# Optimization experiments

Hardware: AMD Instinct MI355X
Metric: run time of the kernel (lower is better)

The kernel has to match this reference:

```python
import jax, jax.numpy as jnp
import numpy as np

B, S, DIM = 1, 2048, 2048
H = 16
Q_LORA, KV_LORA = 1536, 512
D_NOPE, D_ROPE, D_V = 128, 64, 128
D_QK = D_NOPE + D_ROPE  # 192
EPS = 1e-6


def rms_norm(x, w, eps=EPS):
    var = jnp.mean(jnp.square(x), axis=-1, keepdims=True)
    return x * jax.lax.rsqrt(var + eps) * w


def apply_rope(x, cos, sin):
    # x: [B,S,H,D] with interleaved complex pairs; cos/sin: [S,D//2]
    x1, x2 = x[..., 0::2], x[..., 1::2]
    c = cos[None, :, None, :]
    s = sin[None, :, None, :]
    o1 = x1 * c - x2 * s
    o2 = x1 * s + x2 * c
    return jnp.stack([o1, o2], axis=-1).reshape(x.shape)


def setup_inputs() -> dict:
    key = jax.random.key(0)
    ks = jax.random.split(key, 8)
    x = jax.random.normal(ks[0], (B, S, DIM), dtype=jnp.float32)
    # rotary tables (standard complex exponentials)
    inv_freq = 1.0 / (10000.0 ** (np.arange(0, D_ROPE, 2, dtype=np.float32) / D_ROPE))
    t = np.arange(S, dtype=np.float32)
    freqs = np.outer(t, inv_freq)  # [S, D_ROPE//2]
    freqs_cos = jnp.asarray(np.cos(freqs))
    freqs_sin = jnp.asarray(np.sin(freqs))
    sd = lambda fan_in: 1.0 / np.sqrt(fan_in)
    wq_a = jax.random.normal(ks[1], (Q_LORA, DIM), dtype=jnp.float32) * sd(DIM)
    q_a_ln_w = jnp.ones((Q_LORA,), dtype=jnp.float32)
    wq_b = jax.random.normal(ks[2], (H * D_QK, Q_LORA), dtype=jnp.float32) * sd(Q_LORA)
    wkv_a = jax.random.normal(ks[3], (KV_LORA + D_ROPE, DIM), dtype=jnp.float32) * sd(DIM)
    kv_a_ln_w = jnp.ones((KV_LORA,), dtype=jnp.float32)
    wkv_b = jax.random.normal(ks[4], (H * (D_NOPE + D_V), KV_LORA), dtype=jnp.float32) * sd(KV_LORA)
    wo = jax.random.normal(ks[5], (DIM, H * D_V), dtype=jnp.float32) * sd(H * D_V)
    return {"x": x, "freqs_cos": freqs_cos, "freqs_sin": freqs_sin,
            "wq_a": wq_a, "q_a_ln_w": q_a_ln_w, "wq_b": wq_b,
            "wkv_a": wkv_a, "kv_a_ln_w": kv_a_ln_w, "wkv_b": wkv_b, "wo": wo}


def reference(x, freqs_cos, freqs_sin, wq_a, q_a_ln_w, wq_b, wkv_a, kv_a_ln_w, wkv_b, wo):
    softmax_scale = D_QK ** -0.5
    # Query: low-rank down-proj -> RMSNorm -> up-proj
    q = rms_norm(x @ wq_a.T, q_a_ln_w) @ wq_b.T            # [B,S,H*D_QK]
    q = q.reshape(B, S, H, D_QK)
    q_nope, q_pe = q[..., :D_NOPE], q[..., D_NOPE:]
    q_pe = apply_rope(q_pe, freqs_cos, freqs_sin)
    # KV: shared low-rank latent + decoupled rope key (MQA-style, 1 head)
    kv = x @ wkv_a.T                                        # [B,S,KV_LORA+D_ROPE]
    kv_c = rms_norm(kv[..., :KV_LORA], kv_a_ln_w)           # [B,S,KV_LORA]
    k_pe = apply_rope(kv[..., None, KV_LORA:], freqs_cos, freqs_sin)  # [B,S,1,D_ROPE]
    kvb = (kv_c @ wkv_b.T).reshape(B, S, H, D_NOPE + D_V)
    k_nope, v = kvb[..., :D_NOPE], kvb[..., D_NOPE:]
    # Attention scores: nope part + shared rope part
    scores = (jnp.einsum('bqhd,bkhd->bhqk', q_nope, k_nope)
              + jnp.einsum('bqhd,bkd->bhqk', q_pe, k_pe[:, :, 0, :])) * softmax_scale
    causal = jnp.tril(jnp.ones((S, S), dtype=bool))
    scores = jnp.where(causal[None, None], scores, -jnp.inf)
    p = jax.nn.softmax(scores, axis=-1)
    out = jnp.einsum('bhqk,bkhd->bqhd', p, v).reshape(B, S, H * D_V)
    return out @ wo.T
```

## Files before the change

kernel.cpp:

```cpp
#include <hip/hip_runtime.h>
#include <cstdint>
#include <cstddef>

typedef __bf16 bf16;
typedef bf16 bf16x8 __attribute__((ext_vector_type(8)));
typedef bf16 bf16x4 __attribute__((ext_vector_type(4)));
typedef float f32x4 __attribute__((ext_vector_type(4)));

typedef __attribute__((address_space(1))) void as1_void;
typedef __attribute__((address_space(3))) void as3_void;

#define INF __builtin_inff()

__global__ __launch_bounds__(256) void z100_cast_all(
    const float* __restrict__ x, const float* __restrict__ wq_a,
    const float* __restrict__ wkv_a, const float* __restrict__ wq_b,
    const float* __restrict__ wkv_b, const float* __restrict__ wo,
    bf16* __restrict__ x_bf, bf16* __restrict__ wab_bf,
    bf16* __restrict__ wqb_bf, bf16* __restrict__ wkvb_bf,
    bf16* __restrict__ wo_bf) {
    int i = blockIdx.x * 256 + threadIdx.x;
    const float* s;
    bf16* d;
    if (i < 1048576)      { s = x + (size_t)i * 4;                     d = x_bf + (size_t)i * 4; }
    else if (i < 1835008) { int o = i - 1048576; s = wq_a  + (size_t)o * 4; d = wab_bf + (size_t)o * 4; }
    else if (i < 2129920) { int o = i - 1835008; s = wkv_a + (size_t)o * 4; d = wab_bf + 1536ull * 2048 + (size_t)o * 4; }
    else if (i < 3309568) { int o = i - 2129920; s = wq_b  + (size_t)o * 4; d = wqb_bf + (size_t)o * 4; }
    else if (i < 3833856) { int o = i - 3309568; s = wkv_b + (size_t)o * 4; d = wkvb_bf + (size_t)o * 4; }
    else if (i < 4882432) { int o = i - 3833856; s = wo    + (size_t)o * 4; d = wo_bf + (size_t)o * 4; }
    else {                  int o = i - 4882432; bf16x4 z = {};
                            *(bf16x4*)(wab_bf + 2112ull * 2048 + (size_t)o * 4) = z; return; }
    float4 v = *(const float4*)s;
    bf16x4 ovec = { (bf16)v.x, (bf16)v.y, (bf16)v.z, (bf16)v.w };
    *(bf16x4*)d = ovec;
}

__global__ __launch_bounds__(256) void z100_rmsnorm(
    const float* __restrict__ x, int ldx, const float* __restrict__ w,
    bf16* __restrict__ y, int N, float invN) {
    const int row = blockIdx.x;
    const float* xr = x + (size_t)row * ldx;
    float ss = 0.f;
    for (int i = threadIdx.x * 4; i < N; i += 1024) {
        float4 v = *(const float4*)(xr + i);
        ss += v.x * v.x + v.y * v.y + v.z * v.z + v.w * v.w;
    }
    #pragma unroll
    for (int d = 1; d < 64; d <<= 1) ss += __shfl_xor(ss, d);
    __shared__ float red[4];
    if ((threadIdx.x & 63) == 0) red[threadIdx.x >> 6] = ss;
    __syncthreads();
    float tot = red[0] + red[1] + red[2] + red[3];
    float rs = rsqrtf(tot * invN + 1e-6f);
    bf16* yr = y + (size_t)row * N;
    for (int i = threadIdx.x * 4; i < N; i += 1024) {
        float4 v = *(const float4*)(xr + i);
        float4 wv = *(const float4*)(w + i);
        bf16x4 o = { (bf16)(v.x * rs * wv.x), (bf16)(v.y * rs * wv.y),
                     (bf16)(v.z * rs * wv.z), (bf16)(v.w * rs * wv.w) };
        *(bf16x4*)(yr + i) = o;
    }
}

template <typename OutT>
__device__ __forceinline__ void gemm8_body(
    const bf16* __restrict__ A, const bf16* __restrict__ B,
    OutT* __restrict__ C, int N, int K, int ldc, int mblk, int nblk,
    bf16* AsB, bf16* BsB) {
    const int tid = threadIdx.x;
    const int lane = tid & 63, wave = tid >> 6;
    const int l15 = lane & 15, l4 = lane >> 4;
    const int m0 = mblk * 128, n0 = nblk * 128;
    const int wr = (wave >> 1) * 32, wc = (wave & 1) * 64;

    f32x4 acc[2][4] = {};

    const int srow = lane >> 2;
    const int scol = (lane & 3) * 8;
    const size_t a_base = (size_t)(m0 + wave * 16 + srow) * K + scol;
    const size_t b_base = (size_t)(n0 + wave * 16 + srow) * K + scol;

    auto stg = [&](int buf, int k0) {
        __builtin_amdgcn_global_load_lds((as1_void*)(void*)(A + a_base + k0),
                                         (as3_void*)(AsB + buf * 4096 + wave * 512), 16, 0, 0);
        __builtin_amdgcn_global_load_lds((as1_void*)(void*)(B + b_base + k0),
                                         (as3_void*)(BsB + buf * 4096 + wave * 512), 16, 0, 0);
    };

    const int nt = K >> 5;
    stg(0, 0);
    stg(1, 32);
    asm volatile("s_waitcnt vmcnt(2)" ::: "memory");
    __builtin_amdgcn_s_barrier();

    int cb = 0, sb = 2;
    for (int t = 0; t < nt; ++t) {
        if (t + 2 < nt) stg(sb, (t + 2) * 32);
        const bf16* Ab = AsB + cb * 4096;
        const bf16* Bb = BsB + cb * 4096;
        bf16x8 fa[2], fb[4];
        #pragma unroll
        for (int i = 0; i < 2; ++i)
            fa[i] = *(const bf16x8*)(Ab + (wr + 16 * i + l15) * 32 + 8 * l4);
        #pragma unroll
        for (int j = 0; j < 4; ++j)
            fb[j] = *(const bf16x8*)(Bb + (wc + 16 * j + l15) * 32 + 8 * l4);
        #pragma unroll
        for (int i = 0; i < 2; ++i)
            #pragma unroll
            for (int j = 0; j < 4; ++j)
                acc[i][j] = __builtin_amdgcn_mfma_f32_16x16x32_bf16(fa[i], fb[j], acc[i][j], 0, 0, 0);
        if (t + 2 < nt) { asm volatile("s_waitcnt vmcnt(2)" ::: "memory"); }
        else            { asm volatile("s_waitcnt vmcnt(0)" ::: "memory"); }
        __builtin_amdgcn_s_barrier();
        cb = (cb == 2) ? 0 : cb + 1;
        sb = (sb == 2) ? 0 : sb + 1;
    }

    #pragma unroll
    for (int i = 0; i < 2; ++i) {
        int row0 = m0 + wr + 16 * i + 4 * l4;
        #pragma unroll
        for (int j = 0; j < 4; ++j) {
            int col = n0 + wc + 16 * j + l15;
            if (col < N) {
                #pragma unroll
                for (int jj = 0; jj < 4; ++jj)
                    C[(size_t)(row0 + jj) * ldc + col] = (OutT)acc[i][j][jj];
            }
        }
    }
}

__global__ __launch_bounds__(512) void z100_gemm8(
    const bf16* __restrict__ A, const bf16* __restrict__ B,
    float* __restrict__ C, int N, int K, int ldc) {
    __shared__ alignas(16) bf16 As[3 * 128 * 32];
    __shared__ alignas(16) bf16 Bs[3 * 128 * 32];
    gemm8_body<float>(A, B, C, N, K, ldc, blockIdx.y, blockIdx.x, As, Bs);
}

__global__ __launch_bounds__(512) void z100_gemm_qkv(
    const bf16* __restrict__ qan, const bf16* __restrict__ wqb, bf16* __restrict__ qf,
    const bf16* __restrict__ kvc, const bf16* __restrict__ wkvb, bf16* __restrict__ kvbf) {
    __shared__ alignas(16) bf16 As[3 * 128 * 32];
    __shared__ alignas(16) bf16 Bs[3 * 128 * 32];
    const int bid = blockIdx.x;
    if (bid < 384) gemm8_body<bf16>(qan, wqb, qf, 3072, 1536, 3072, bid / 24, bid % 24, As, Bs);
    else { int b = bid - 384; gemm8_body<bf16>(kvc, wkvb, kvbf, 4096, 512, 4096, b / 32, b % 32, As, Bs); }
}

__global__ void z100_qk_prep(const bf16* __restrict__ q,
                             const bf16* __restrict__ kvb, const float* __restrict__ kpe,
                             int kpe_ld,
                             const float* __restrict__ fc, const float* __restrict__ fs,
                             bf16* __restrict__ q_attn, bf16* __restrict__ k_attn) {
    const int TOT = 2048 * 16 * 96;
    int u = blockIdx.x * 256 + threadIdx.x;
    if (u < TOT) {
        int e = u % 96;
        int sh = u / 96;
        int h = sh % 16, s = sh / 16;
        const float scale = 0.072168783649f;
        const bf16* qp = q + (size_t)s * 3072 + h * 192;
        bf16* o = q_attn + ((size_t)h * 2048 + s) * 192;
        if (e < 64) {
            o[2 * e]     = (bf16)((float)qp[2 * e] * scale);
            o[2 * e + 1] = (bf16)((float)qp[2 * e + 1] * scale);
        } else {
            int i = e - 64;
            float c = fc[s * 32 + i], sn = fs[s * 32 + i];
            float x1 = (float)qp[128 + 2 * i], x2 = (float)qp[128 + 2 * i + 1];
            o[128 + 2 * i]     = (bf16)((x1 * c - x2 * sn) * scale);
            o[128 + 2 * i + 1] = (bf16)((x1 * sn + x2 * c) * scale);
        }
    } else {
        u -= TOT;
        int e = u % 96;
        int sh = u / 96;
        int h = sh % 16, s = sh / 16;
        bf16* o = k_attn + ((size_t)h * 2048 + s) * 192;
        if (e < 64) {
            const bf16* kp = kvb + (size_t)s * 4096 + h * 256;
            o[2 * e]     = kp[2 * e];
            o[2 * e + 1] = kp[2 * e + 1];
        } else {
            int i = e - 64;
            float c = fc[s * 32 + i], sn = fs[s * 32 + i];
            float x1 = kpe[(size_t)s * kpe_ld + 2 * i];
            float x2 = kpe[(size_t)s * kpe_ld + 2 * i + 1];
            o[128 + 2 * i]     = (bf16)(x1 * c - x2 * sn);
            o[128 + 2 * i + 1] = (bf16)(x1 * sn + x2 * c);
        }
    }
}

__global__ __launch_bounds__(256) void z100_v_trans(const bf16* __restrict__ kvb,
                                                    bf16* __restrict__ vt) {
    const int st = blockIdx.x, h = blockIdx.y;
    const int s0 = st * 64;
    __shared__ alignas(16) bf16 tile[64 * 132];
    const int tid = threadIdx.x;
    #pragma unroll
    for (int i = 0; i < 4; ++i) {
        int slot = i * 256 + tid;
        int r = slot >> 4, c8 = slot & 15;
        bf16x8 v = *(const bf16x8*)(kvb + (size_t)(s0 + r) * 4096 + h * 256 + 128 + c8 * 8);
        *(bf16x8*)(tile + r * 132 + c8 * 8) = v;
    }
    __syncthreads();
    #pragma unroll
    for (int i = 0; i < 4; ++i) {
        int slot = i * 256 + tid;
        int d = slot >> 3, ch = slot & 7;
        bf16x8 o;
        #pragma unroll
        for (int j = 0; j < 8; ++j) o[j] = tile[(ch * 8 + j) * 132 + d];
        *(bf16x8*)(vt + ((size_t)h * 128 + d) * 2048 + s0 + ch * 8) = o;
    }
}

__global__ __launch_bounds__(512) void z100_attn(
    const bf16* __restrict__ q_attn, const bf16* __restrict__ k_attn,
    const bf16* __restrict__ v_t, bf16* __restrict__ opart, float* __restrict__ ml) {
    const int bid = blockIdx.x;
    const int wk = (bid & 7) * 80 + (bid >> 3);
    const int h = wk / 40;
    const int s0w = wk - h * 40;
    int qt = 0, rem = s0w;
    while (rem >= (qt >> 2) + 1) { rem -= (qt >> 2) + 1; ++qt; }
    const int chk = rem;
    const int q0 = qt * 128;
    const int kstart = chk * 512;
    const int kend = min(q0 + 128, kstart + 512);
    const int slot = h * 40 + s0w;

    const int tid = threadIdx.x;
    const int lane = tid & 63, wave = tid >> 6;
    const int l15 = lane & 15, l4 = lane >> 4;

    __shared__ alignas(16) bf16 Ks[2][64 * 192];
    __shared__ alignas(16) bf16 Vs[2][128 * 64];

    const bf16* Qh = q_attn + (size_t)h * 2048 * 192;
    const bf16* Kh = k_attn + (size_t)h * 2048 * 192;
    const bf16* Vh = v_t + (size_t)h * 128 * 2048;

    const int wrow_max = q0 + wave * 16 + 15;
    const int diag_k0 = q0 + (wave >> 2) * 64;

    bf16x8 qf[6];
    {
        const bf16* qr = Qh + (size_t)(q0 + wave * 16 + l15) * 192 + 8 * l4;
        #pragma unroll
        for (int c = 0; c < 6; ++c) qf[c] = *(const bf16x8*)(qr + 32 * c);
    }

    int koff[3], voff[2];
    #pragma unroll
    for (int i = 0; i < 3; ++i) {
        int off = (wave * 3 + i) * 1024 + lane * 16;
        int r = off / 384;
        int ch = (off % 384) >> 4;
        int ksrc = (r & 0x23) | ((r & 0x0C) << 1) | ((r & 0x10) >> 2);
        koff[i] = ksrc * 192 + (ch ^ (r & 7)) * 8;
    }
    #pragma unroll
    for (int i = 0; i < 2; ++i) {
        int off = (wave * 2 + i) * 1024 + lane * 16;
        int d = off >> 7;
        int ch = (off >> 4) & 7;
        voff[i] = d * 2048 + (ch ^ (d & 7)) * 8;
    }

    auto stage = [&](int buf, int k0) {
        #pragma unroll
        for (int i = 0; i < 3; ++i)
            __builtin_amdgcn_global_load_lds(
                (as1_void*)(void*)(Kh + (size_t)k0 * 192 + koff[i]),
                (as3_void*)((char*)&Ks[buf][0] + (wave * 3 + i) * 1024), 16, 0, 0);
        #pragma unroll
        for (int i = 0; i < 2; ++i)
            __builtin_amdgcn_global_load_lds(
                (as1_void*)(void*)(Vh + k0 + voff[i]),
                (as3_void*)((char*)&Vs[buf][0] + (wave * 2 + i) * 1024), 16, 0, 0);
    };

    f32x4 oacc[8] = {};
    float m_r = -INF, l_r = 0.f;
    const int nt = (kend - kstart) >> 6;

    stage(0, kstart);
    __syncthreads();
    int cur = 0;
    for (int t = 0; t < nt; ++t) {
        const int k0 = kstart + t * 64;
        if (t + 1 < nt) stage(cur ^ 1, k0 + 64);

        if (k0 <= wrow_max) {
            const char* KsC = (const char*)&Ks[cur][0];
            const char* VsC = (const char*)&Vs[cur][0];

            f32x4 sc[4];
            __builtin_amdgcn_s_setprio(1);
            #pragma unroll
            for (int kt = 0; kt < 4; ++kt) {
                f32x4 a = { 0.f, 0.f, 0.f, 0.f };
                int r = 16 * kt + l15;
                #pragma unroll
                for (int c = 0; c < 6; ++c) {
                    int byteo = (r * 384 + c * 64 + l4 * 16) ^ ((r & 7) << 4);
                    bf16x8 kf = *(const bf16x8*)(KsC + byteo);
                    a = __builtin_amdgcn_mfma_f32_16x16x32_bf16(kf, qf[c], a, 0, 0, 0);
                }
                sc[kt] = a;
            }
            __builtin_amdgcn_s_setprio(0);

            if (k0 == diag_k0) {
                int qrow = (wave & 3) * 16 + l15;
                #pragma unroll
                for (int kt = 0; kt < 4; ++kt)
                    #pragma unroll
                    for (int r = 0; r < 4; ++r) {
                        int kl = ((kt >> 1) << 5) | (l4 << 3) | ((kt & 1) << 2) | r;
                        if (kl > qrow) sc[kt][r] = -INF;
                    }
            }

            float mx = -INF;
            #pragma unroll
            for (int kt = 0; kt < 4; ++kt)
                #pragma unroll
                for (int r = 0; r < 4; ++r) mx = fmaxf(mx, sc[kt][r]);
            mx = fmaxf(mx, __shfl_xor(mx, 16));
            mx = fmaxf(mx, __shfl_xor(mx, 32));
            float mnew = fmaxf(m_r, mx);
            float corr = __expf(m_r - mnew);
            float rs = 0.f;
            #pragma unroll
            for (int kt = 0; kt < 4; ++kt)
                #pragma unroll
                for (int r = 0; r < 4; ++r) {
                    float pv = __expf(sc[kt][r] - mnew);
                    sc[kt][r] = pv;
                    rs += pv;
                }
            rs += __shfl_xor(rs, 16);
            rs += __shfl_xor(rs, 32);
            l_r = l_r * corr + rs;
            m_r = mnew;

            float c_r[4];
            #pragma unroll
            for (int r = 0; r < 4; ++r) c_r[r] = __shfl(corr, 20 * l4 + r);
            #pragma unroll
            for (int dt = 0; dt < 8; ++dt)
                #pragma unroll
                for (int r = 0; r < 4; ++r) oacc[dt][r] *= c_r[r];

            bf16x8 pf[2];
            #pragma unroll
            for (int c2 = 0; c2 < 2; ++c2)
                #pragma unroll
                for (int i = 0; i < 8; ++i)
                    pf[c2][i] = (bf16)sc[2 * c2 + (i >> 2)][i & 3];

            __builtin_amdgcn_s_setprio(1);
            #pragma unroll
            for (int dt = 0; dt < 8; ++dt) {
                #pragma unroll
                for (int c2 = 0; c2 < 2; ++c2) {
                    int d = 16 * dt + l15;
                    int byteo = (d * 128 + c2 * 64 + l4 * 16) ^ ((d & 7) << 4);
                    bf16x8 vf = *(const bf16x8*)(VsC + byteo);
                    oacc[dt] = __builtin_amdgcn_mfma_f32_16x16x32_bf16(pf[c2], vf, oacc[dt], 0, 0, 0);
                }
            }
            __builtin_amdgcn_s_setprio(0);
        }

        __syncthreads();
        cur ^= 1;
    }

    const int qr_base = wave * 16;
    if (lane < 16) {
        ml[(size_t)slot * 256 + qr_base + lane] = m_r;
        ml[(size_t)slot * 256 + 128 + qr_base + lane] = l_r;
    }
    bf16* ob = opart + (size_t)slot * 16384;
    #pragma unroll
    for (int dt = 0; dt < 8; ++dt) {
        int d = 16 * dt + l15;
        #pragma unroll
        for (int r = 0; r < 4; ++r) {
            int qr = qr_base + 4 * l4 + r;
            ob[qr * 128 + d] = (bf16)oacc[dt][r];
        }
    }
}

__global__ __launch_bounds__(512) void z100_attn_combine(
    const bf16* __restrict__ opart, const float* __restrict__ ml, bf16* __restrict__ ao) {
    const int qt = blockIdx.x, h = blockIdx.y;
    const int t = threadIdx.x;
    const int np = (qt >> 2) + 1;
    int base = 0;
    for (int j = 0; j < qt; ++j) base += (j >> 2) + 1;
    const int slot0 = h * 40 + base;
    #pragma unroll 1
    for (int it = 0; it < 4; ++it) {
        const int c = it * 512 + t;
        const int qr = c >> 4;
        const int dc = (c & 15) * 8;
        float m[4], l[4], w[4];
        float M = -INF;
        #pragma unroll
        for (int i = 0; i < 4; ++i)
            if (i < np) {
                m[i] = ml[(size_t)(slot0 + i) * 256 + qr];
                l[i] = ml[(size_t)(slot0 + i) * 256 + 128 + qr];
                M = fmaxf(M, m[i]);
            }
        float L = 0.f;
        #pragma unroll
        for (int i = 0; i < 4; ++i)
            if (i < np) {
                w[i] = __expf(m[i] - M);
                L += w[i] * l[i];
            }
        float invL = 1.f / L;
        float acc[8] = {};
        #pragma unroll
        for (int i = 0; i < 4; ++i)
            if (i < np) {
                bf16x8 a = *(const bf16x8*)(opart + (size_t)(slot0 + i) * 16384 + (size_t)c * 8);
                #pragma unroll
                for (int j = 0; j < 8; ++j) acc[j] += w[i] * (float)a[j];
            }
        bf16x8 o;
        #pragma unroll
        for (int j = 0; j < 8; ++j) o[j] = (bf16)(acc[j] * invL);
        *(bf16x8*)(ao + (size_t)(qt * 128 + qr) * 2048 + h * 128 + dc) = o;
    }
}

extern "C" void kernel_launch(void* const* d_in, const int* in_sizes, int n_in,
                              void* d_out, int out_size, void* d_ws, size_t ws_size,
                              hipStream_t stream) {
    (void)in_sizes; (void)n_in; (void)out_size; (void)ws_size;
    const float* x     = (const float*)d_in[0];
    const float* fc    = (const float*)d_in[1];
    const float* fs    = (const float*)d_in[2];
    const float* wq_a  = (const float*)d_in[3];
    const float* q_ln  = (const float*)d_in[4];
    const float* wq_b  = (const float*)d_in[5];
    const float* wkv_a = (const float*)d_in[6];
    const float* kv_ln = (const float*)d_in[7];
    const float* wkv_b = (const float*)d_in[8];
    const float* wo    = (const float*)d_in[9];
    float* out = (float*)d_out;

    char* p = (char*)d_ws;
    auto alloc = [&](size_t bytes) {
        char* r = p;
        p += (bytes + 255) & ~(size_t)255;
        return r;
    };
    char* phase1  = p;
    bf16* x_bf    = (bf16*)alloc(2048ull * 2048 * 2);
    bf16* wab_bf  = (bf16*)alloc(2176ull * 2048 * 2);
    float* qa_f   = (float*)alloc(2048ull * 2112 * 4);
    bf16* qan_bf  = (bf16*)alloc(2048ull * 1536 * 2);
    bf16* wqb_bf  = (bf16*)alloc(3072ull * 1536 * 2);
    bf16* wkvb_bf = (bf16*)alloc(4096ull * 512 * 2);
    bf16* wo_bf   = (bf16*)alloc(2048ull * 2048 * 2);
    bf16* q_f     = (bf16*)alloc(2048ull * 3072 * 2);
    bf16* kvc_bf  = (bf16*)alloc(2048ull * 512 * 2);
    bf16* kvb_f   = (bf16*)alloc(2048ull * 4096 * 2);
    bf16* q_attn  = (bf16*)alloc(16ull * 2048 * 192 * 2);
    bf16* k_attn  = (bf16*)alloc(16ull * 2048 * 192 * 2);
    bf16* v_t     = (bf16*)alloc(16ull * 128 * 2048 * 2);
    bf16* ao_bf   = (bf16*)alloc(2048ull * 2048 * 2);
    bf16* opart   = (bf16*)phase1;
    float* mlbuf  = (float*)(phase1 + 640ull * 16384 * 2);

    z100_cast_all<<<19200, 256, 0, stream>>>(x, wq_a, wkv_a, wq_b, wkv_b, wo,
                                             x_bf, wab_bf, wqb_bf, wkvb_bf, wo_bf);

    z100_gemm8<<<dim3(17, 16), 512, 0, stream>>>(x_bf, wab_bf, qa_f, 2112, 2048, 2112);
    z100_rmsnorm<<<2048, 256, 0, stream>>>(qa_f, 2112, q_ln, qan_bf, 1536, 1.f / 1536.f);
    z100_rmsnorm<<<2048, 256, 0, stream>>>(qa_f + 1536, 2112, kv_ln, kvc_bf, 512, 1.f / 512.f);

    z100_gemm_qkv<<<dim3(896), 512, 0, stream>>>(qan_bf, wqb_bf, q_f, kvc_bf, wkvb_bf, kvb_f);

    z100_qk_prep<<<24576, 256, 0, stream>>>(q_f, kvb_f, qa_f + 2048, 2112, fc, fs, q_attn, k_attn);
    z100_v_trans<<<dim3(32, 16), 256, 0, stream>>>(kvb_f, v_t);

    z100_attn<<<dim3(640), 512, 0, stream>>>(q_attn, k_attn, v_t, opart, mlbuf);
    z100_attn_combine<<<dim3(16, 16), 512, 0, stream>>>(opart, mlbuf, ao_bf);

    z100_gemm8<<<dim3(16, 16), 512, 0, stream>>>(ao_bf, wo_bf, out, 2048, 2048, 2048);
}
```

Baseline: 236.7 us.

## Read Q/K directly from projection outputs, fold softmax scale into wq_b

Removes the full q_attn/k_attn repacking. The attention kernel now loads Q-nope and K-nope straight from the GEMM outputs, and only small rope buffers (qpe, kpe) are built. The softmax scale is folded into wq_b during the weight cast. The first projection writes bf16 instead of fp32, and rmsnorm reads bf16. This cuts intermediate memory traffic and prep-kernel work, at the cost of strided K loads with a 4096-element row stride and extra bf16 rounding before the norm and rope.

```diff
diff --git a/kernel.cpp b/kernel.cpp
--- a/kernel.cpp
+++ b/kernel.cpp
@@ -22,28 +22,31 @@
     int i = blockIdx.x * 256 + threadIdx.x;
     const float* s;
     bf16* d;
+    float mul = 1.f;
     if (i < 1048576)      { s = x + (size_t)i * 4;                     d = x_bf + (size_t)i * 4; }
     else if (i < 1835008) { int o = i - 1048576; s = wq_a  + (size_t)o * 4; d = wab_bf + (size_t)o * 4; }
     else if (i < 2129920) { int o = i - 1835008; s = wkv_a + (size_t)o * 4; d = wab_bf + 1536ull * 2048 + (size_t)o * 4; }
-    else if (i < 3309568) { int o = i - 2129920; s = wq_b  + (size_t)o * 4; d = wqb_bf + (size_t)o * 4; }
+    else if (i < 3309568) { int o = i - 2129920; s = wq_b  + (size_t)o * 4; d = wqb_bf + (size_t)o * 4;
+                            mul = 0.072168783649f; }
     else if (i < 3833856) { int o = i - 3309568; s = wkv_b + (size_t)o * 4; d = wkvb_bf + (size_t)o * 4; }
     else if (i < 4882432) { int o = i - 3833856; s = wo    + (size_t)o * 4; d = wo_bf + (size_t)o * 4; }
     else {                  int o = i - 4882432; bf16x4 z = {};
                             *(bf16x4*)(wab_bf + 2112ull * 2048 + (size_t)o * 4) = z; return; }
     float4 v = *(const float4*)s;
-    bf16x4 ovec = { (bf16)v.x, (bf16)v.y, (bf16)v.z, (bf16)v.w };
+    bf16x4 ovec = { (bf16)(v.x * mul), (bf16)(v.y * mul), (bf16)(v.z * mul), (bf16)(v.w * mul) };
     *(bf16x4*)d = ovec;
 }
 
-__global__ __launch_bounds__(256) void z100_rmsnorm(
-    const float* __restrict__ x, int ldx, const float* __restrict__ w,
+__global__ __launch_bounds__(256) void z100_rmsnorm_bf(
+    const bf16* __restrict__ x, int ldx, const float* __restrict__ w,
     bf16* __restrict__ y, int N, float invN) {
     const int row = blockIdx.x;
-    const float* xr = x + (size_t)row * ldx;
+    const bf16* xr = x + (size_t)row * ldx;
     float ss = 0.f;
-    for (int i = threadIdx.x * 4; i < N; i += 1024) {
-        float4 v = *(const float4*)(xr + i);
-        ss += v.x * v.x + v.y * v.y + v.z * v.z + v.w * v.w;
+    for (int i = threadIdx.x * 8; i < N; i += 2048) {
+        bf16x8 v = *(const bf16x8*)(xr + i);
+        #pragma unroll
+        for (int j = 0; j < 8; ++j) { float f = (float)v[j]; ss += f * f; }
     }
     #pragma unroll
     for (int d = 1; d < 64; d <<= 1) ss += __shfl_xor(ss, d);
@@ -53,12 +56,16 @@
     float tot = red[0] + red[1] + red[2] + red[3];
     float rs = rsqrtf(tot * invN + 1e-6f);
     bf16* yr = y + (size_t)row * N;
-    for (int i = threadIdx.x * 4; i < N; i += 1024) {
-        float4 v = *(const float4*)(xr + i);
-        float4 wv = *(const float4*)(w + i);
-        bf16x4 o = { (bf16)(v.x * rs * wv.x), (bf16)(v.y * rs * wv.y),
-                     (bf16)(v.z * rs * wv.z), (bf16)(v.w * rs * wv.w) };
-        *(bf16x4*)(yr + i) = o;
+    for (int i = threadIdx.x * 8; i < N; i += 2048) {
+        bf16x8 v = *(const bf16x8*)(xr + i);
+        float4 w0 = *(const float4*)(w + i);
+        float4 w1 = *(const float4*)(w + i + 4);
+        bf16x8 o;
+        o[0] = (bf16)((float)v[0] * rs * w0.x); o[1] = (bf16)((float)v[1] * rs * w0.y);
+        o[2] = (bf16)((float)v[2] * rs * w0.z); o[3] = (bf16)((float)v[3] * rs * w0.w);
+        o[4] = (bf16)((float)v[4] * rs * w1.x); o[5] = (bf16)((float)v[5] * rs * w1.y);
+        o[6] = (bf16)((float)v[6] * rs * w1.z); o[7] = (bf16)((float)v[7] * rs * w1.w);
+        *(bf16x8*)(yr + i) = o;
     }
 }
 
@@ -140,6 +147,14 @@
     gemm8_body<float>(A, B, C, N, K, ldc, blockIdx.y, blockIdx.x, As, Bs);
 }
 
+__global__ __launch_bounds__(512) void z100_gemm8_bf(
+    const bf16* __restrict__ A, const bf16* __restrict__ B,
+    bf16* __restrict__ C, int N, int K, int ldc) {
+    __shared__ alignas(16) bf16 As[3 * 128 * 32];
+    __shared__ alignas(16) bf16 Bs[3 * 128 * 32];
+    gemm8_body<bf16>(A, B, C, N, K, ldc, blockIdx.y, blockIdx.x, As, Bs);
+}
+
 __global__ __launch_bounds__(512) void z100_gemm_qkv(
     const bf16* __restrict__ qan, const bf16* __restrict__ wqb, bf16* __restrict__ qf,
     const bf16* __restrict__ kvc, const bf16* __restrict__ wkvb, bf16* __restrict__ kvbf) {
@@ -150,48 +165,29 @@
     else { int b = bid - 384; gemm8_body<bf16>(kvc, wkvb, kvbf, 4096, 512, 4096, b / 32, b % 32, As, Bs); }
 }
 
-__global__ void z100_qk_prep(const bf16* __restrict__ q,
-                             const bf16* __restrict__ kvb, const float* __restrict__ kpe,
-                             int kpe_ld,
+__global__ void z100_pe_prep(const bf16* __restrict__ q_f, const bf16* __restrict__ qa,
                              const float* __restrict__ fc, const float* __restrict__ fs,
-                             bf16* __restrict__ q_attn, bf16* __restrict__ k_attn) {
-    const int TOT = 2048 * 16 * 96;
+                             bf16* __restrict__ qpe, bf16* __restrict__ kpe) {
+    const int QTOT = 2048 * 16 * 32;
     int u = blockIdx.x * 256 + threadIdx.x;
-    if (u < TOT) {
-        int e = u % 96;
-        int sh = u / 96;
-        int h = sh % 16, s = sh / 16;
-        const float scale = 0.072168783649f;
-        const bf16* qp = q + (size_t)s * 3072 + h * 192;
-        bf16* o = q_attn + ((size_t)h * 2048 + s) * 192;
-        if (e < 64) {
-            o[2 * e]     = (bf16)((float)qp[2 * e] * scale);
-            o[2 * e + 1] = (bf16)((float)qp[2 * e + 1] * scale);
-        } else {
-            int i = e - 64;
-            float c = fc[s * 32 + i], sn = fs[s * 32 + i];
-            float x1 = (float)qp[128 + 2 * i], x2 = (float)qp[128 + 2 * i + 1];
-            o[128 + 2 * i]     = (bf16)((x1 * c - x2 * sn) * scale);
-            o[128 + 2 * i + 1] = (bf16)((x1 * sn + x2 * c) * scale);
-        }
+    if (u < QTOT) {
+        int i = u & 31;
+        int h = (u >> 5) & 15;
+        int s = u >> 9;
+        float c = fc[s * 32 + i], sn = fs[s * 32 + i];
+        float x1 = (float)q_f[(size_t)s * 3072 + h * 192 + 128 + 2 * i];
+        float x2 = (float)q_f[(size_t)s * 3072 + h * 192 + 128 + 2 * i + 1];
+        qpe[(size_t)s * 1024 + h * 64 + 2 * i]     = (bf16)(x1 * c - x2 * sn);
+        qpe[(size_t)s * 1024 + h * 64 + 2 * i + 1] = (bf16)(x1 * sn + x2 * c);
     } else {
-        u -= TOT;
-        int e = u % 96;
-        int sh = u / 96;
-        int h = sh % 16, s = sh / 16;
-        bf16* o = k_attn + ((size_t)h * 2048 + s) * 192;
-        if (e < 64) {
-            const bf16* kp = kvb + (size_t)s * 4096 + h * 256;
-            o[2 * e]     = kp[2 * e];
-            o[2 * e + 1] = kp[2 * e + 1];
-        } else {
-            int i = e - 64;
-            float c = fc[s * 32 + i], sn = fs[s * 32 + i];
-            float x1 = kpe[(size_t)s * kpe_ld + 2 * i];
-            float x2 = kpe[(size_t)s * kpe_ld + 2 * i + 1];
-            o[128 + 2 * i]     = (bf16)(x1 * c - x2 * sn);
-            o[128 + 2 * i + 1] = (bf16)(x1 * sn + x2 * c);
-        }
+        int v = u - QTOT;
+        int i = v & 31;
+        int s = v >> 5;
+        float c = fc[s * 32 + i], sn = fs[s * 32 + i];
+        float x1 = (float)qa[(size_t)s * 2112 + 2048 + 2 * i];
+        float x2 = (float)qa[(size_t)s * 2112 + 2048 + 2 * i + 1];
+        kpe[(size_t)s * 64 + 2 * i]     = (bf16)(x1 * c - x2 * sn);
+        kpe[(size_t)s * 64 + 2 * i + 1] = (bf16)(x1 * sn + x2 * c);
     }
 }
 
@@ -221,7 +217,8 @@
 }
 
 __global__ __launch_bounds__(512) void z100_attn(
-    const bf16* __restrict__ q_attn, const bf16* __restrict__ k_attn,
+    const bf16* __restrict__ q_f, const bf16* __restrict__ qpe,
+    const bf16* __restrict__ kvb, const bf16* __restrict__ kpe,
     const bf16* __restrict__ v_t, bf16* __restrict__ opart, float* __restrict__ ml) {
     const int bid = blockIdx.x;
     const int wk = (bid & 7) * 80 + (bid >> 3);
@@ -242,8 +239,6 @@
     __shared__ alignas(16) bf16 Ks[2][64 * 192];
     __shared__ alignas(16) bf16 Vs[2][128 * 64];
 
-    const bf16* Qh = q_attn + (size_t)h * 2048 * 192;
-    const bf16* Kh = k_attn + (size_t)h * 2048 * 192;
     const bf16* Vh = v_t + (size_t)h * 128 * 2048;
 
     const int wrow_max = q0 + wave * 16 + 15;
@@ -251,20 +246,28 @@
 
     bf16x8 qf[6];
     {
-        const bf16* qr = Qh + (size_t)(q0 + wave * 16 + l15) * 192 + 8 * l4;
-        #pragma unroll
-        for (int c = 0; c < 6; ++c) qf[c] = *(const bf16x8*)(qr + 32 * c);
-    }
-
-    int koff[3], voff[2];
+        const int qrow = q0 + wave * 16 + l15;
+        const bf16* qn = q_f + (size_t)qrow * 3072 + h * 192 + 8 * l4;
+        #pragma unroll
+        for (int c = 0; c < 4; ++c) qf[c] = *(const bf16x8*)(qn + 32 * c);
+        const bf16* qp = qpe + (size_t)qrow * 1024 + h * 64 + 8 * l4;
+        qf[4] = *(const bf16x8*)(qp);
+        qf[5] = *(const bf16x8*)(qp + 32);
+    }
+
+    const bf16* kp0[3];
+    int kstep[3];
     #pragma unroll
     for (int i = 0; i < 3; ++i) {
         int off = (wave * 3 + i) * 1024 + lane * 16;
         int r = off / 384;
         int ch = (off % 384) >> 4;
         int ksrc = (r & 0x23) | ((r & 0x0C) << 1) | ((r & 0x10) >> 2);
-        koff[i] = ksrc * 192 + (ch ^ (r & 7)) * 8;
-    }
+        int chx = ch ^ (r & 7);
+        if (chx < 16) { kp0[i] = kvb + (size_t)ksrc * 4096 + h * 256 + chx * 8; kstep[i] = 4096; }
+        else          { kp0[i] = kpe + (size_t)ksrc * 64 + (chx - 16) * 8;      kstep[i] = 64; }
+    }
+    int voff[2];
     #pragma unroll
     for (int i = 0; i < 2; ++i) {
         int off = (wave * 2 + i) * 1024 + lane * 16;
@@ -277,7 +280,7 @@
         #pragma unroll
         for (int i = 0; i < 3; ++i)
             __builtin_amdgcn_global_load_lds(
-                (as1_void*)(void*)(Kh + (size_t)k0 * 192 + koff[i]),
+                (as1_void*)(void*)(kp0[i] + (size_t)k0 * kstep[i]),
                 (as3_void*)((char*)&Ks[buf][0] + (wave * 3 + i) * 1024), 16, 0, 0);
         #pragma unroll
         for (int i = 0; i < 2; ++i)
@@ -471,7 +474,7 @@
     char* phase1  = p;
     bf16* x_bf    = (bf16*)alloc(2048ull * 2048 * 2);
     bf16* wab_bf  = (bf16*)alloc(2176ull * 2048 * 2);
-    float* qa_f   = (float*)alloc(2048ull * 2112 * 4);
+    bf16* qa_bf   = (bf16*)alloc(2048ull * 2112 * 2);
     bf16* qan_bf  = (bf16*)alloc(2048ull * 1536 * 2);
     bf16* wqb_bf  = (bf16*)alloc(3072ull * 1536 * 2);
     bf16* wkvb_bf = (bf16*)alloc(4096ull * 512 * 2);
@@ -479,8 +482,8 @@
     bf16* q_f     = (bf16*)alloc(2048ull * 3072 * 2);
     bf16* kvc_bf  = (bf16*)alloc(2048ull * 512 * 2);
     bf16* kvb_f   = (bf16*)alloc(2048ull * 4096 * 2);
-    bf16* q_attn  = (bf16*)alloc(16ull * 2048 * 192 * 2);
-    bf16* k_attn  = (bf16*)alloc(16ull * 2048 * 192 * 2);
+    bf16* qpe     = (bf16*)alloc(2048ull * 16 * 64 * 2);
+    bf16* kpe     = (bf16*)alloc(2048ull * 64 * 2);
     bf16* v_t     = (bf16*)alloc(16ull * 128 * 2048 * 2);
     bf16* ao_bf   = (bf16*)alloc(2048ull * 2048 * 2);
     bf16* opart   = (bf16*)phase1;
@@ -489,16 +492,16 @@
     z100_cast_all<<<19200, 256, 0, stream>>>(x, wq_a, wkv_a, wq_b, wkv_b, wo,
                                              x_bf, wab_bf, wqb_bf, wkvb_bf, wo_bf);
 
-    z100_gemm8<<<dim3(17, 16), 512, 0, stream>>>(x_bf, wab_bf, qa_f, 2112, 2048, 2112);
-    z100_rmsnorm<<<2048, 256, 0, stream>>>(qa_f, 2112, q_ln, qan_bf, 1536, 1.f / 1536.f);
-    z100_rmsnorm<<<2048, 256, 0, stream>>>(qa_f + 1536, 2112, kv_ln, kvc_bf, 512, 1.f / 512.f);
+    z100_gemm8_bf<<<dim3(17, 16), 512, 0, stream>>>(x_bf, wab_bf, qa_bf, 2112, 2048, 2112);
+    z100_rmsnorm_bf<<<2048, 256, 0, stream>>>(qa_bf, 2112, q_ln, qan_bf, 1536, 1.f / 1536.f);
+    z100_rmsnorm_bf<<<2048, 256, 0, stream>>>(qa_bf + 1536, 2112, kv_ln, kvc_bf, 512, 1.f / 512.f);
 
     z100_gemm_qkv<<<dim3(896), 512, 0, stream>>>(qan_bf, wqb_bf, q_f, kvc_bf, wkvb_bf, kvb_f);
 
-    z100_qk_prep<<<24576, 256, 0, stream>>>(q_f, kvb_f, qa_f + 2048, 2112, fc, fs, q_attn, k_attn);
+    z100_pe_prep<<<4352, 256, 0, stream>>>(q_f, qa_bf, fc, fs, qpe, kpe);
     z100_v_trans<<<dim3(32, 16), 256, 0, stream>>>(kvb_f, v_t);
 
-    z100_attn<<<dim3(640), 512, 0, stream>>>(q_attn, k_attn, v_t, opart, mlbuf);
+    z100_attn<<<dim3(640), 512, 0, stream>>>(q_f, qpe, kvb_f, kpe, v_t, opart, mlbuf);
     z100_attn_combine<<<dim3(16, 16), 512, 0, stream>>>(opart, mlbuf, ao_bf);
 
     z100_gemm8<<<dim3(16, 16), 512, 0, stream>>>(ao_bf, wo_bf, out, 2048, 2048, 2048);
```

Measured after the change: 224.3 us. 1.06x faster.
